# Kernel optimization log

Hardware: AMD Instinct MI355X
Metric: run time of the kernel (lower is better)

Reference implementation:

```python
import jax, jax.numpy as jnp
import numpy as np

D = 1024      # hidden_size
M = 256       # num_random_features
N = 16384     # number of hidden states
K = 8192      # number of weight rows (HSM nodes)
EPS = 1e-6


def _orthogonal_random_features(key, d, m):
    # m < d: single QR block, first m rows, scaled by sqrt(d)
    rm = jax.random.normal(key, (d, d), dtype=jnp.float32)
    q, _ = jnp.linalg.qr(rm)
    return q[:m] * jnp.sqrt(jnp.float32(d))


def setup_inputs() -> dict:
    key = jax.random.key(0)
    k1, k2, k3 = jax.random.split(key, 3)
    hidden_states = jax.random.normal(k1, (N, D), dtype=jnp.float32)
    weights = jax.random.normal(k2, (K, D), dtype=jnp.float32)
    omega = _orthogonal_random_features(k3, D, M)
    return {"hidden_states": hidden_states, "weights": weights, "omega": omega}


def _positive_random_features(x, omega):
    # phi(x) = (exp(x @ Omega^T - ||x||^2/2 - max) + eps) / sqrt(m)
    projection = x @ omega.T                                  # (..., m)
    x_norm_sq = jnp.sum(x * x, axis=-1, keepdims=True)        # (..., 1)
    exponent = projection - x_norm_sq / 2
    exponent_max = jnp.max(exponent, axis=-1, keepdims=True)
    features = (jnp.exp(exponent - exponent_max) + EPS) / jnp.sqrt(jnp.float32(omega.shape[0]))
    return features, x_norm_sq, exponent_max


def reference(hidden_states, weights, omega):
    # temperature = 1.0 (default), so no input rescaling
    phi_h, h_norm_sq, h_max = _positive_random_features(hidden_states, omega)  # (n,m)
    phi_w, w_norm_sq, w_max = _positive_random_features(weights, omega)        # (k,m)
    rf_kernel = phi_h @ phi_w.T                                                # (n,k)
    log_correction = (h_norm_sq + w_norm_sq.T) / 2 + h_max + w_max.T           # (n,k)
    log_correction = jnp.clip(log_correction, -80.0, 80.0)
    log_rf_kernel = jnp.log(rf_kernel + 1e-10)
    log_exp_approx = jnp.clip(log_rf_kernel + log_correction, -80.0, 80.0)
    exp_approx = jnp.exp(log_exp_approx)
    return exp_approx / (1.0 + exp_approx)
```

## Files before the change

### kernel.cpp

```cpp
#include <hip/hip_runtime.h>

#define DD 1024
#define MM 256
#define NN 16384
#define KK 8192

typedef float f32x4 __attribute__((ext_vector_type(4)));
typedef unsigned int u32x4 __attribute__((ext_vector_type(4)));
typedef unsigned int u32x2 __attribute__((ext_vector_type(2)));
typedef __bf16 bf16x8 __attribute__((ext_vector_type(8)));
typedef unsigned short u16;
typedef unsigned int u32;

static __device__ __forceinline__ u16 f2bf(float f) {
    u32 u = __builtin_bit_cast(u32, f);
    u32 r = u + 0x7fffu + ((u >> 16) & 1u);
    return (u16)(r >> 16);
}
static __device__ __forceinline__ float bf2f(u16 h) {
    u32 u = ((u32)h) << 16;
    return __builtin_bit_cast(float, u);
}

static __device__ __forceinline__ void gload_lds16(const void* g, void* l) {
    __builtin_amdgcn_global_load_lds(
        (const __attribute__((address_space(1))) u32*)g,
        (__attribute__((address_space(3))) u32*)l, 16, 0, 0);
}

static __device__ __forceinline__ bf16x8 ldfrag(const u16* p) {
    return __builtin_bit_cast(bf16x8, *(const u32x4*)p);
}

#define MFMA16(a, b, c) __builtin_amdgcn_mfma_f32_16x16x32_bf16((a), (b), (c), 0, 0, 0)

__global__ void k_conv(const float* __restrict__ om, u16* __restrict__ oh,
                       u16* __restrict__ ol) {
    int i = (blockIdx.x * blockDim.x + threadIdx.x) * 4;
    f32x4 x = *(const f32x4*)(om + i);
    ushort4 h, l;
    u16 t;
    t = f2bf(x.x); h.x = t; l.x = f2bf(x.x - bf2f(t));
    t = f2bf(x.y); h.y = t; l.y = f2bf(x.y - bf2f(t));
    t = f2bf(x.z); h.z = t; l.z = f2bf(x.z - bf2f(t));
    t = f2bf(x.w); h.w = t; l.w = f2bf(x.w - bf2f(t));
    *(ushort4*)(oh + i) = h;
    *(ushort4*)(ol + i) = l;
}

__global__ __launch_bounds__(256, 4)
void k_stageA(const float* __restrict__ Hs, const float* __restrict__ Ws,
              const u16* __restrict__ Oh, const u16* __restrict__ Ol,
              u16* __restrict__ phiH, u16* __restrict__ phiW,
              float* __restrict__ emH, float* __restrict__ emW)
{
    __shared__ alignas(16) u16 Ah[32 * 32];
    __shared__ alignas(16) u16 Al[32 * 32];
    __shared__ alignas(16) u16 Bh[256 * 32];
    __shared__ alignas(16) u16 Bl[256 * 32];
    __shared__ float redmax[4][32];

    const int tid  = threadIdx.x;
    const int lane = tid & 63;
    const int wid  = tid >> 6;

    const float* __restrict__ X;
    u16* __restrict__ phi;
    float* __restrict__ em;
    int row0;
    if (blockIdx.x < NN / 32) {
        X = Hs; phi = phiH; em = emH; row0 = blockIdx.x * 32;
    } else {
        X = Ws; phi = phiW; em = emW; row0 = (blockIdx.x - NN / 32) * 32;
    }

    f32x4 acc[2][4];
#pragma unroll
    for (int m = 0; m < 2; ++m)
#pragma unroll
        for (int n = 0; n < 4; ++n) acc[m][n] = f32x4{0.f, 0.f, 0.f, 0.f};

    const int arow = tid >> 3;
    const int acol = (tid & 7) * 4;
    const float* __restrict__ xrow = X + (long)(row0 + arow) * DD;
    const int a_idx = arow * 32 + (acol ^ (((arow >> 1) & 3) << 3));

    const int r16 = lane & 15;
    const int h8  = (lane >> 4) << 3;
    int aoffs[2], boffs[4];
#pragma unroll
    for (int m = 0; m < 2; ++m) {
        int row = m * 16 + r16;
        aoffs[m] = row * 32 + (h8 ^ (((row >> 1) & 3) << 3));
    }
#pragma unroll
    for (int n = 0; n < 4; ++n) {
        int row = wid * 64 + n * 16 + r16;
        boffs[n] = row * 32 + (h8 ^ (((row >> 1) & 3) << 3));
    }

    for (int ks = 0; ks < DD / 32; ++ks) {
        const int k0 = ks * 32;
#pragma unroll
        for (int s = 0; s < 4; ++s) {
            const int c    = s * 256 + tid;
            const int brow = c >> 2;
            const int scol = k0 + (((c & 3) << 3) ^ (((brow >> 1) & 3) << 3));
            gload_lds16(Oh + brow * DD + scol, Bh + (s * 256 + wid * 64) * 8);
            gload_lds16(Ol + brow * DD + scol, Bl + (s * 256 + wid * 64) * 8);
        }
        f32x4 x = *(const f32x4*)(xrow + k0 + acol);
        u32x2 ph, pl;
#pragma unroll
        for (int j = 0; j < 2; ++j) {
            u16 h0 = f2bf(x[2 * j]);
            u16 h1 = f2bf(x[2 * j + 1]);
            u16 l0 = f2bf(x[2 * j] - bf2f(h0));
            u16 l1 = f2bf(x[2 * j + 1] - bf2f(h1));
            ph[j] = (u32)h0 | ((u32)h1 << 16);
            pl[j] = (u32)l0 | ((u32)l1 << 16);
        }
        *(u32x2*)(Ah + a_idx) = ph;
        *(u32x2*)(Al + a_idx) = pl;
        __syncthreads();

        bf16x8 fah[2], fal[2], fbh[4], fbl[4];
#pragma unroll
        for (int m = 0; m < 2; ++m) {
            fah[m] = ldfrag(Ah + aoffs[m]);
            fal[m] = ldfrag(Al + aoffs[m]);
        }
#pragma unroll
        for (int n = 0; n < 4; ++n) {
            fbh[n] = ldfrag(Bh + boffs[n]);
            fbl[n] = ldfrag(Bl + boffs[n]);
        }
#pragma unroll
        for (int m = 0; m < 2; ++m)
#pragma unroll
            for (int n = 0; n < 4; ++n) {
                acc[m][n] = MFMA16(fah[m], fbh[n], acc[m][n]);
                acc[m][n] = MFMA16(fah[m], fbl[n], acc[m][n]);
                acc[m][n] = MFMA16(fal[m], fbh[n], acc[m][n]);
            }
        __syncthreads();
    }

#pragma unroll
    for (int m = 0; m < 2; ++m) {
#pragma unroll
        for (int i = 0; i < 4; ++i) {
            float v = fmaxf(fmaxf(acc[m][0][i], acc[m][1][i]),
                            fmaxf(acc[m][2][i], acc[m][3][i]));
            v = fmaxf(v, __shfl_xor(v, 1));
            v = fmaxf(v, __shfl_xor(v, 2));
            v = fmaxf(v, __shfl_xor(v, 4));
            v = fmaxf(v, __shfl_xor(v, 8));
            if (r16 == 0) redmax[wid][m * 16 + ((lane >> 4) << 2) + i] = v;
        }
    }
    __syncthreads();
    if (tid < 32) {
        float fm = fmaxf(fmaxf(redmax[0][tid], redmax[1][tid]),
                         fmaxf(redmax[2][tid], redmax[3][tid]));
        em[row0 + tid] = __expf(fminf(fmaxf(-fm, -87.f), 87.f));
    }
#pragma unroll
    for (int m = 0; m < 2; ++m) {
#pragma unroll
        for (int i = 0; i < 4; ++i) {
            const int rl = m * 16 + ((lane >> 4) << 2) + i;
            const float fm = fmaxf(fmaxf(redmax[0][rl], redmax[1][rl]),
                                   fmaxf(redmax[2][rl], redmax[3][rl]));
#pragma unroll
            for (int n = 0; n < 4; ++n) {
                float p   = acc[m][n][i];
                float ph_ = (__expf(p - fm) + 1e-6f) * 0.0625f;
                phi[(long)(row0 + rl) * MM + wid * 64 + n * 16 + r16] = f2bf(ph_);
            }
        }
    }
}

__global__ __launch_bounds__(256, 3)
void k_stageB(const u16* __restrict__ PH, const u16* __restrict__ PW,
              const float* __restrict__ EH, const float* __restrict__ EW,
              float* __restrict__ out)
{
    __shared__ alignas(16) u16 As[128 * 64];
    __shared__ alignas(16) u16 Bs[128 * 64];

    const int tid  = threadIdx.x;
    const int lane = tid & 63;
    const int wid  = tid >> 6;
    const int bm   = blockIdx.x >> 6;
    const int bn   = blockIdx.x & 63;
    const int row0 = bm * 128, col0 = bn * 128;
    const int wr   = wid >> 1, wc = wid & 1;
    const int r16  = lane & 15;
    const int h8   = (lane >> 4) << 3;

    f32x4 acc[4][4];
#pragma unroll
    for (int m = 0; m < 4; ++m)
#pragma unroll
        for (int n = 0; n < 4; ++n) acc[m][n] = f32x4{0.f, 0.f, 0.f, 0.f};

    int aoffs[2][4], boffs[2][4];
#pragma unroll
    for (int sl = 0; sl < 2; ++sl) {
#pragma unroll
        for (int m = 0; m < 4; ++m) {
            int row = wr * 64 + m * 16 + r16;
            aoffs[sl][m] = row * 64 + (((((sl * 32 + h8) << 1)) ^ ((row & 7) << 4)) >> 1);
        }
#pragma unroll
        for (int n = 0; n < 4; ++n) {
            int row = wc * 64 + n * 16 + r16;
            boffs[sl][n] = row * 64 + (((((sl * 32 + h8) << 1)) ^ ((row & 7) << 4)) >> 1);
        }
    }

    for (int ks = 0; ks < 4; ++ks) {
        const int k0 = ks * 64;
#pragma unroll
        for (int s = 0; s < 4; ++s) {
            const int c    = s * 256 + tid;
            const int row  = c >> 3;
            const int cbl  = ((c & 7) << 4) ^ ((row & 7) << 4);
            const int scol = k0 + (cbl >> 1);
            gload_lds16(PH + (long)(row0 + row) * MM + scol, As + (s * 256 + wid * 64) * 8);
            gload_lds16(PW + (long)(col0 + row) * MM + scol, Bs + (s * 256 + wid * 64) * 8);
        }
        __syncthreads();
#pragma unroll
        for (int sl = 0; sl < 2; ++sl) {
            bf16x8 fa[4], fb[4];
#pragma unroll
            for (int m = 0; m < 4; ++m) fa[m] = ldfrag(As + aoffs[sl][m]);
#pragma unroll
            for (int n = 0; n < 4; ++n) fb[n] = ldfrag(Bs + boffs[sl][n]);
#pragma unroll
            for (int m = 0; m < 4; ++m)
#pragma unroll
                for (int n = 0; n < 4; ++n)
                    acc[m][n] = MFMA16(fa[m], fb[n], acc[m][n]);
        }
        __syncthreads();
    }

    float ew_[4];
#pragma unroll
    for (int n = 0; n < 4; ++n) ew_[n] = EW[col0 + wc * 64 + n * 16 + r16];

#pragma unroll
    for (int m = 0; m < 4; ++m) {
#pragma unroll
        for (int i = 0; i < 4; ++i) {
            const int row = row0 + wr * 64 + m * 16 + ((lane >> 4) << 2) + i;
            const float eh = EH[row];
#pragma unroll
            for (int n = 0; n < 4; ++n) {
                float rf = acc[m][n][i] + 1e-10f;
                float t  = eh * ew_[n];
                float o  = rf * __builtin_amdgcn_rcpf(rf + t);
                __builtin_nontemporal_store(
                    o, &out[(long)row * KK + col0 + wc * 64 + n * 16 + r16]);
            }
        }
    }
}

extern "C" void kernel_launch(void* const* d_in, const int* in_sizes, int n_in,
                              void* d_out, int out_size, void* d_ws, size_t ws_size,
                              hipStream_t stream) {
    (void)in_sizes; (void)n_in; (void)out_size; (void)ws_size;
    const float* H  = (const float*)d_in[0];
    const float* W  = (const float*)d_in[1];
    const float* Om = (const float*)d_in[2];
    float* out = (float*)d_out;

    char* ws   = (char*)d_ws;
    u16*  phiH = (u16*)ws;
    u16*  phiW = (u16*)(ws + (size_t)NN * MM * 2);
    float* emh = (float*)(ws + (size_t)(NN + KK) * MM * 2);
    float* emw = emh + NN;
    u16*  oh   = (u16*)(emw + KK);
    u16*  ol   = oh + MM * DD;

    k_conv<<<(MM * DD) / 1024, 256, 0, stream>>>(Om, oh, ol);
    k_stageA<<<(NN + KK) / 32, 256, 0, stream>>>(H, W, oh, ol, phiH, phiW, emh, emw);
    k_stageB<<<(NN / 128) * (KK / 128), 256, 0, stream>>>(phiH, phiW, emh, emw, out);
}
```

Baseline: 196.3 us.

## Double-buffer both GEMM stages, load A fragments directly, swizzle stage B tiles

Stage A now double-buffers the omega tiles in LDS and prefetches the next hidden-state slice into registers while the current one is computed. The hidden rows are split to bf16 hi/lo directly into MFMA fragments without an LDS round trip, and hidden-state blocks cover 64 rows instead of 32. Stage B double-buffers its LDS tiles so global loads overlap the MFMAs, and remaps block indices so concurrently running blocks share rows for L2 reuse. Both kernels lower their launch_bounds occupancy hint to 2 and use more LDS per block, trading occupancy for overlap.

```diff
diff --git a/kernel.cpp b/kernel.cpp
--- a/kernel.cpp
+++ b/kernel.cpp
@@ -7,7 +7,6 @@
 
 typedef float f32x4 __attribute__((ext_vector_type(4)));
 typedef unsigned int u32x4 __attribute__((ext_vector_type(4)));
-typedef unsigned int u32x2 __attribute__((ext_vector_type(2)));
 typedef __bf16 bf16x8 __attribute__((ext_vector_type(8)));
 typedef unsigned short u16;
 typedef unsigned int u32;
@@ -48,106 +47,115 @@
     *(ushort4*)(ol + i) = l;
 }
 
-__global__ __launch_bounds__(256, 4)
-void k_stageA(const float* __restrict__ Hs, const float* __restrict__ Ws,
-              const u16* __restrict__ Oh, const u16* __restrict__ Ol,
-              u16* __restrict__ phiH, u16* __restrict__ phiW,
-              float* __restrict__ emH, float* __restrict__ emW)
+template<int MT>
+static __device__ __forceinline__ void stageA_body(
+    const float* __restrict__ X,
+    const u16* __restrict__ Oh, const u16* __restrict__ Ol,
+    u16* __restrict__ phi, float* __restrict__ em, int row0,
+    u16* __restrict__ Bh0, u16* __restrict__ Bl0,
+    u16* __restrict__ Bh1, u16* __restrict__ Bl1,
+    float (*redmax)[64])
 {
-    __shared__ alignas(16) u16 Ah[32 * 32];
-    __shared__ alignas(16) u16 Al[32 * 32];
-    __shared__ alignas(16) u16 Bh[256 * 32];
-    __shared__ alignas(16) u16 Bl[256 * 32];
-    __shared__ float redmax[4][32];
-
     const int tid  = threadIdx.x;
     const int lane = tid & 63;
     const int wid  = tid >> 6;
-
-    const float* __restrict__ X;
-    u16* __restrict__ phi;
-    float* __restrict__ em;
-    int row0;
-    if (blockIdx.x < NN / 32) {
-        X = Hs; phi = phiH; em = emH; row0 = blockIdx.x * 32;
-    } else {
-        X = Ws; phi = phiW; em = emW; row0 = (blockIdx.x - NN / 32) * 32;
-    }
-
-    f32x4 acc[2][4];
-#pragma unroll
-    for (int m = 0; m < 2; ++m)
+    const int r16  = lane & 15;
+    const int h8   = (lane >> 4) << 3;
+
+    f32x4 acc[MT][4];
+#pragma unroll
+    for (int m = 0; m < MT; ++m)
 #pragma unroll
         for (int n = 0; n < 4; ++n) acc[m][n] = f32x4{0.f, 0.f, 0.f, 0.f};
 
-    const int arow = tid >> 3;
-    const int acol = (tid & 7) * 4;
-    const float* __restrict__ xrow = X + (long)(row0 + arow) * DD;
-    const int a_idx = arow * 32 + (acol ^ (((arow >> 1) & 3) << 3));
-
-    const int r16 = lane & 15;
-    const int h8  = (lane >> 4) << 3;
-    int aoffs[2], boffs[4];
-#pragma unroll
-    for (int m = 0; m < 2; ++m) {
-        int row = m * 16 + r16;
-        aoffs[m] = row * 32 + (h8 ^ (((row >> 1) & 3) << 3));
-    }
+    int boffs[4];
 #pragma unroll
     for (int n = 0; n < 4; ++n) {
         int row = wid * 64 + n * 16 + r16;
         boffs[n] = row * 32 + (h8 ^ (((row >> 1) & 3) << 3));
     }
 
-    for (int ks = 0; ks < DD / 32; ++ks) {
+    const float* xb[MT];
+#pragma unroll
+    for (int m = 0; m < MT; ++m)
+        xb[m] = X + (long)(row0 + m * 16 + r16) * DD + h8;
+
+    u32x4 xr0[MT][2], xr1[MT][2];
+
+    auto stage = [&](int ks, u16* bh, u16* bl) {
         const int k0 = ks * 32;
 #pragma unroll
         for (int s = 0; s < 4; ++s) {
             const int c    = s * 256 + tid;
             const int brow = c >> 2;
             const int scol = k0 + (((c & 3) << 3) ^ (((brow >> 1) & 3) << 3));
-            gload_lds16(Oh + brow * DD + scol, Bh + (s * 256 + wid * 64) * 8);
-            gload_lds16(Ol + brow * DD + scol, Bl + (s * 256 + wid * 64) * 8);
-        }
-        f32x4 x = *(const f32x4*)(xrow + k0 + acol);
-        u32x2 ph, pl;
-#pragma unroll
-        for (int j = 0; j < 2; ++j) {
-            u16 h0 = f2bf(x[2 * j]);
-            u16 h1 = f2bf(x[2 * j + 1]);
-            u16 l0 = f2bf(x[2 * j] - bf2f(h0));
-            u16 l1 = f2bf(x[2 * j + 1] - bf2f(h1));
-            ph[j] = (u32)h0 | ((u32)h1 << 16);
-            pl[j] = (u32)l0 | ((u32)l1 << 16);
-        }
-        *(u32x2*)(Ah + a_idx) = ph;
-        *(u32x2*)(Al + a_idx) = pl;
-        __syncthreads();
-
-        bf16x8 fah[2], fal[2], fbh[4], fbl[4];
-#pragma unroll
-        for (int m = 0; m < 2; ++m) {
-            fah[m] = ldfrag(Ah + aoffs[m]);
-            fal[m] = ldfrag(Al + aoffs[m]);
+            gload_lds16(Oh + brow * DD + scol, bh + (s * 256 + wid * 64) * 8);
+            gload_lds16(Ol + brow * DD + scol, bl + (s * 256 + wid * 64) * 8);
+        }
+    };
+    auto loadA = [&](int ks, u32x4 (&xr)[MT][2]) {
+        const int k0 = ks * 32;
+#pragma unroll
+        for (int m = 0; m < MT; ++m) {
+            xr[m][0] = *(const u32x4*)(xb[m] + k0);
+            xr[m][1] = *(const u32x4*)(xb[m] + k0 + 4);
+        }
+    };
+    auto compute = [&](u32x4 (&xr)[MT][2], const u16* bh, const u16* bl) {
+        bf16x8 fah[MT], fal[MT], fbh[4], fbl[4];
+#pragma unroll
+        for (int m = 0; m < MT; ++m) {
+            f32x4 a = __builtin_bit_cast(f32x4, xr[m][0]);
+            f32x4 b = __builtin_bit_cast(f32x4, xr[m][1]);
+            const float p0[4] = {a[0], a[2], b[0], b[2]};
+            const float p1[4] = {a[1], a[3], b[1], b[3]};
+            u32x4 ph, pl;
+#pragma unroll
+            for (int j = 0; j < 4; ++j) {
+                u16 h0 = f2bf(p0[j]);
+                u16 h1 = f2bf(p1[j]);
+                u16 l0 = f2bf(p0[j] - bf2f(h0));
+                u16 l1 = f2bf(p1[j] - bf2f(h1));
+                ph[j] = (u32)h0 | ((u32)h1 << 16);
+                pl[j] = (u32)l0 | ((u32)l1 << 16);
+            }
+            fah[m] = __builtin_bit_cast(bf16x8, ph);
+            fal[m] = __builtin_bit_cast(bf16x8, pl);
         }
 #pragma unroll
         for (int n = 0; n < 4; ++n) {
-            fbh[n] = ldfrag(Bh + boffs[n]);
-            fbl[n] = ldfrag(Bl + boffs[n]);
-        }
-#pragma unroll
-        for (int m = 0; m < 2; ++m)
+            fbh[n] = ldfrag(bh + boffs[n]);
+            fbl[n] = ldfrag(bl + boffs[n]);
+        }
+#pragma unroll
+        for (int m = 0; m < MT; ++m)
 #pragma unroll
             for (int n = 0; n < 4; ++n) {
                 acc[m][n] = MFMA16(fah[m], fbh[n], acc[m][n]);
                 acc[m][n] = MFMA16(fah[m], fbl[n], acc[m][n]);
                 acc[m][n] = MFMA16(fal[m], fbh[n], acc[m][n]);
             }
+    };
+
+    stage(0, Bh0, Bl0);
+    loadA(0, xr0);
+    __syncthreads();
+
+    for (int ks = 0; ks < 32; ks += 2) {
+        stage(ks + 1, Bh1, Bl1);
+        loadA(ks + 1, xr1);
+        compute(xr0, Bh0, Bl0);
         __syncthreads();
-    }
-
-#pragma unroll
-    for (int m = 0; m < 2; ++m) {
+        if (ks + 2 < 32) {
+            stage(ks + 2, Bh0, Bl0);
+            loadA(ks + 2, xr0);
+        }
+        compute(xr1, Bh1, Bl1);
+        __syncthreads();
+    }
+
+#pragma unroll
+    for (int m = 0; m < MT; ++m)
 #pragma unroll
         for (int i = 0; i < 4; ++i) {
             float v = fmaxf(fmaxf(acc[m][0][i], acc[m][1][i]),
@@ -158,15 +166,14 @@
             v = fmaxf(v, __shfl_xor(v, 8));
             if (r16 == 0) redmax[wid][m * 16 + ((lane >> 4) << 2) + i] = v;
         }
-    }
     __syncthreads();
-    if (tid < 32) {
+    if (tid < MT * 16) {
         float fm = fmaxf(fmaxf(redmax[0][tid], redmax[1][tid]),
                          fmaxf(redmax[2][tid], redmax[3][tid]));
         em[row0 + tid] = __expf(fminf(fmaxf(-fm, -87.f), 87.f));
     }
 #pragma unroll
-    for (int m = 0; m < 2; ++m) {
+    for (int m = 0; m < MT; ++m)
 #pragma unroll
         for (int i = 0; i < 4; ++i) {
             const int rl = m * 16 + ((lane >> 4) << 2) + i;
@@ -179,22 +186,39 @@
                 phi[(long)(row0 + rl) * MM + wid * 64 + n * 16 + r16] = f2bf(ph_);
             }
         }
-    }
-}
-
-__global__ __launch_bounds__(256, 3)
+}
+
+__global__ __launch_bounds__(256, 2)
+void k_stageA(const float* __restrict__ Hs, const float* __restrict__ Ws,
+              const u16* __restrict__ Oh, const u16* __restrict__ Ol,
+              u16* __restrict__ phiH, u16* __restrict__ phiW,
+              float* __restrict__ emH, float* __restrict__ emW)
+{
+    __shared__ alignas(16) u16 Bh[2][256 * 32];
+    __shared__ alignas(16) u16 Bl[2][256 * 32];
+    __shared__ float redmax[4][64];
+    if (blockIdx.x < NN / 64)
+        stageA_body<4>(Hs, Oh, Ol, phiH, emH, blockIdx.x * 64,
+                       Bh[0], Bl[0], Bh[1], Bl[1], redmax);
+    else
+        stageA_body<2>(Ws, Oh, Ol, phiW, emW, (blockIdx.x - NN / 64) * 32,
+                       Bh[0], Bl[0], Bh[1], Bl[1], redmax);
+}
+
+__global__ __launch_bounds__(256, 2)
 void k_stageB(const u16* __restrict__ PH, const u16* __restrict__ PW,
               const float* __restrict__ EH, const float* __restrict__ EW,
               float* __restrict__ out)
 {
-    __shared__ alignas(16) u16 As[128 * 64];
-    __shared__ alignas(16) u16 Bs[128 * 64];
+    __shared__ alignas(16) u16 As[2][128 * 64];
+    __shared__ alignas(16) u16 Bs[2][128 * 64];
 
     const int tid  = threadIdx.x;
     const int lane = tid & 63;
     const int wid  = tid >> 6;
-    const int bm   = blockIdx.x >> 6;
-    const int bn   = blockIdx.x & 63;
+    const int swz  = (blockIdx.x & 7) * 1024 + (blockIdx.x >> 3);
+    const int bm   = swz >> 6;
+    const int bn   = swz & 63;
     const int row0 = bm * 128, col0 = bn * 128;
     const int wr   = wid >> 1, wc = wid & 1;
     const int r16  = lane & 15;
@@ -212,34 +236,43 @@
 #pragma unroll
         for (int m = 0; m < 4; ++m) {
             int row = wr * 64 + m * 16 + r16;
-            aoffs[sl][m] = row * 64 + (((((sl * 32 + h8) << 1)) ^ ((row & 7) << 4)) >> 1);
+            aoffs[sl][m] = row * 64 + ((sl * 32 + h8) ^ ((row & 7) << 3));
         }
 #pragma unroll
         for (int n = 0; n < 4; ++n) {
             int row = wc * 64 + n * 16 + r16;
-            boffs[sl][n] = row * 64 + (((((sl * 32 + h8) << 1)) ^ ((row & 7) << 4)) >> 1);
-        }
-    }
-
-    for (int ks = 0; ks < 4; ++ks) {
+            boffs[sl][n] = row * 64 + ((sl * 32 + h8) ^ ((row & 7) << 3));
+        }
+    }
+
+    auto stage = [&](int ks, int b) {
         const int k0 = ks * 64;
 #pragma unroll
         for (int s = 0; s < 4; ++s) {
             const int c    = s * 256 + tid;
             const int row  = c >> 3;
-            const int cbl  = ((c & 7) << 4) ^ ((row & 7) << 4);
-            const int scol = k0 + (cbl >> 1);
-            gload_lds16(PH + (long)(row0 + row) * MM + scol, As + (s * 256 + wid * 64) * 8);
-            gload_lds16(PW + (long)(col0 + row) * MM + scol, Bs + (s * 256 + wid * 64) * 8);
-        }
-        __syncthreads();
+            const int scol = k0 + (((c & 7) << 3) ^ ((row & 7) << 3));
+            gload_lds16(PH + (long)(row0 + row) * MM + scol,
+                        &As[b][(s * 256 + wid * 64) * 8]);
+            gload_lds16(PW + (long)(col0 + row) * MM + scol,
+                        &Bs[b][(s * 256 + wid * 64) * 8]);
+        }
+    };
+
+    stage(0, 0);
+    __syncthreads();
+
+#pragma unroll
+    for (int ks = 0; ks < 4; ++ks) {
+        const int b = ks & 1;
+        if (ks < 3) stage(ks + 1, b ^ 1);
 #pragma unroll
         for (int sl = 0; sl < 2; ++sl) {
             bf16x8 fa[4], fb[4];
 #pragma unroll
-            for (int m = 0; m < 4; ++m) fa[m] = ldfrag(As + aoffs[sl][m]);
-#pragma unroll
-            for (int n = 0; n < 4; ++n) fb[n] = ldfrag(Bs + boffs[sl][n]);
+            for (int m = 0; m < 4; ++m) fa[m] = ldfrag(&As[b][0] + aoffs[sl][m]);
+#pragma unroll
+            for (int n = 0; n < 4; ++n) fb[n] = ldfrag(&Bs[b][0] + boffs[sl][n]);
 #pragma unroll
             for (int m = 0; m < 4; ++m)
 #pragma unroll
@@ -289,6 +322,6 @@
     u16*  ol   = oh + MM * DD;
 
     k_conv<<<(MM * DD) / 1024, 256, 0, stream>>>(Om, oh, ol);
-    k_stageA<<<(NN + KK) / 32, 256, 0, stream>>>(H, W, oh, ol, phiH, phiW, emh, emw);
+    k_stageA<<<NN / 64 + KK / 32, 256, 0, stream>>>(H, W, oh, ol, phiH, phiW, emh, emw);
     k_stageB<<<(NN / 128) * (KK / 128), 256, 0, stream>>>(phiH, phiW, emh, emw, out);
 }
```

New measurement: 253.1 us. 1.29x slower.

## Make stage A per-wave with register-prefetched X and no block barriers

Applied to the files above, without the earlier changes.

Stage A now gives each wave a private LDS slice of the omega tile and loads the hidden-state A fragments straight from global memory into registers, splitting them into bf16 hi/lo there. Nothing is shared between waves, so the two __syncthreads per K-step go away. The next step's omega tile and X values are prefetched into a double-buffered register set before the current step's MFMAs are issued. The cost is more registers, so launch bounds drop from 4 to 3 waves, and each wave now reads X on its own. The correctness of the in-place LDS reuse depends on the hand-placed s_waitcnt ordering.

```diff
diff --git a/kernel.cpp b/kernel.cpp
--- a/kernel.cpp
+++ b/kernel.cpp
@@ -7,7 +7,6 @@
 
 typedef float f32x4 __attribute__((ext_vector_type(4)));
 typedef unsigned int u32x4 __attribute__((ext_vector_type(4)));
-typedef unsigned int u32x2 __attribute__((ext_vector_type(2)));
 typedef __bf16 bf16x8 __attribute__((ext_vector_type(8)));
 typedef unsigned short u16;
 typedef unsigned int u32;
@@ -48,21 +47,21 @@
     *(ushort4*)(ol + i) = l;
 }
 
-__global__ __launch_bounds__(256, 4)
+__global__ __launch_bounds__(256, 3)
 void k_stageA(const float* __restrict__ Hs, const float* __restrict__ Ws,
               const u16* __restrict__ Oh, const u16* __restrict__ Ol,
               u16* __restrict__ phiH, u16* __restrict__ phiW,
               float* __restrict__ emH, float* __restrict__ emW)
 {
-    __shared__ alignas(16) u16 Ah[32 * 32];
-    __shared__ alignas(16) u16 Al[32 * 32];
-    __shared__ alignas(16) u16 Bh[256 * 32];
-    __shared__ alignas(16) u16 Bl[256 * 32];
+    __shared__ alignas(16) u16 BhS[4][64 * 32];
+    __shared__ alignas(16) u16 BlS[4][64 * 32];
     __shared__ float redmax[4][32];
 
     const int tid  = threadIdx.x;
     const int lane = tid & 63;
     const int wid  = tid >> 6;
+    const int r16  = lane & 15;
+    const int h8   = (lane >> 4) << 3;
 
     const float* __restrict__ X;
     u16* __restrict__ phi;
@@ -80,60 +79,78 @@
 #pragma unroll
         for (int n = 0; n < 4; ++n) acc[m][n] = f32x4{0.f, 0.f, 0.f, 0.f};
 
-    const int arow = tid >> 3;
-    const int acol = (tid & 7) * 4;
-    const float* __restrict__ xrow = X + (long)(row0 + arow) * DD;
-    const int a_idx = arow * 32 + (acol ^ (((arow >> 1) & 3) << 3));
-
-    const int r16 = lane & 15;
-    const int h8  = (lane >> 4) << 3;
-    int aoffs[2], boffs[4];
-#pragma unroll
-    for (int m = 0; m < 2; ++m) {
-        int row = m * 16 + r16;
-        aoffs[m] = row * 32 + (h8 ^ (((row >> 1) & 3) << 3));
-    }
+    u16* const mybh = &BhS[wid][0];
+    u16* const mybl = &BlS[wid][0];
+
+    int boffs[4];
 #pragma unroll
     for (int n = 0; n < 4; ++n) {
-        int row = wid * 64 + n * 16 + r16;
-        boffs[n] = row * 32 + (h8 ^ (((row >> 1) & 3) << 3));
-    }
-
-    for (int ks = 0; ks < DD / 32; ++ks) {
-        const int k0 = ks * 32;
+        int rl = n * 16 + r16;
+        boffs[n] = rl * 32 + (h8 ^ (((rl >> 1) & 3) << 3));
+    }
+
+    const u16* srch[4];
+    const u16* srcl[4];
+#pragma unroll
+    for (int s = 0; s < 4; ++s) {
+        int rl  = s * 16 + (lane >> 2);
+        int col = ((lane & 3) << 3) ^ (((rl >> 1) & 3) << 3);
+        srch[s] = Oh + (long)(wid * 64 + rl) * DD + col;
+        srcl[s] = Ol + (long)(wid * 64 + rl) * DD + col;
+    }
+
+    const float* xb[2];
+#pragma unroll
+    for (int m = 0; m < 2; ++m)
+        xb[m] = X + (long)(row0 + m * 16 + r16) * DD + h8;
+
+    u32x4 xrA[2][2], xrB[2][2];
+
+    auto stageO = [&](int k0) {
 #pragma unroll
         for (int s = 0; s < 4; ++s) {
-            const int c    = s * 256 + tid;
-            const int brow = c >> 2;
-            const int scol = k0 + (((c & 3) << 3) ^ (((brow >> 1) & 3) << 3));
-            gload_lds16(Oh + brow * DD + scol, Bh + (s * 256 + wid * 64) * 8);
-            gload_lds16(Ol + brow * DD + scol, Bl + (s * 256 + wid * 64) * 8);
-        }
-        f32x4 x = *(const f32x4*)(xrow + k0 + acol);
-        u32x2 ph, pl;
-#pragma unroll
-        for (int j = 0; j < 2; ++j) {
-            u16 h0 = f2bf(x[2 * j]);
-            u16 h1 = f2bf(x[2 * j + 1]);
-            u16 l0 = f2bf(x[2 * j] - bf2f(h0));
-            u16 l1 = f2bf(x[2 * j + 1] - bf2f(h1));
-            ph[j] = (u32)h0 | ((u32)h1 << 16);
-            pl[j] = (u32)l0 | ((u32)l1 << 16);
-        }
-        *(u32x2*)(Ah + a_idx) = ph;
-        *(u32x2*)(Al + a_idx) = pl;
-        __syncthreads();
-
-        bf16x8 fah[2], fal[2], fbh[4], fbl[4];
+            gload_lds16(srch[s] + k0, mybh + s * 512);
+            gload_lds16(srcl[s] + k0, mybl + s * 512);
+        }
+    };
+    auto loadX = [&](int k0, u32x4 (&xr)[2][2]) {
 #pragma unroll
         for (int m = 0; m < 2; ++m) {
-            fah[m] = ldfrag(Ah + aoffs[m]);
-            fal[m] = ldfrag(Al + aoffs[m]);
-        }
+            xr[m][0] = *(const u32x4*)(xb[m] + k0);
+            xr[m][1] = *(const u32x4*)(xb[m] + k0 + 4);
+        }
+    };
+    auto step = [&](u32x4 (&xr)[2][2], u32x4 (&xrn)[2][2], int k_next) {
+        asm volatile("s_waitcnt vmcnt(0)" ::: "memory");
+        bf16x8 fbh[4], fbl[4];
 #pragma unroll
         for (int n = 0; n < 4; ++n) {
-            fbh[n] = ldfrag(Bh + boffs[n]);
-            fbl[n] = ldfrag(Bl + boffs[n]);
+            fbh[n] = ldfrag(mybh + boffs[n]);
+            fbl[n] = ldfrag(mybl + boffs[n]);
+        }
+        bf16x8 fah[2], fal[2];
+#pragma unroll
+        for (int m = 0; m < 2; ++m) {
+            f32x4 a = __builtin_bit_cast(f32x4, xr[m][0]);
+            f32x4 b = __builtin_bit_cast(f32x4, xr[m][1]);
+            const float e[8] = {a[0], a[1], a[2], a[3], b[0], b[1], b[2], b[3]};
+            u32x4 ph, pl;
+#pragma unroll
+            for (int j = 0; j < 4; ++j) {
+                u16 h0 = f2bf(e[2 * j]);
+                u16 h1 = f2bf(e[2 * j + 1]);
+                u16 l0 = f2bf(e[2 * j] - bf2f(h0));
+                u16 l1 = f2bf(e[2 * j + 1] - bf2f(h1));
+                ph[j] = (u32)h0 | ((u32)h1 << 16);
+                pl[j] = (u32)l0 | ((u32)l1 << 16);
+            }
+            fah[m] = __builtin_bit_cast(bf16x8, ph);
+            fal[m] = __builtin_bit_cast(bf16x8, pl);
+        }
+        asm volatile("s_waitcnt lgkmcnt(0)" ::: "memory");
+        if (k_next < DD) {
+            stageO(k_next);
+            loadX(k_next, xrn);
         }
 #pragma unroll
         for (int m = 0; m < 2; ++m)
@@ -143,11 +160,18 @@
                 acc[m][n] = MFMA16(fah[m], fbl[n], acc[m][n]);
                 acc[m][n] = MFMA16(fal[m], fbh[n], acc[m][n]);
             }
-        __syncthreads();
-    }
-
-#pragma unroll
-    for (int m = 0; m < 2; ++m) {
+    };
+
+    stageO(0);
+    loadX(0, xrA);
+
+    for (int ks = 0; ks < 32; ks += 2) {
+        step(xrA, xrB, (ks + 1) * 32);
+        step(xrB, xrA, (ks + 2) * 32);
+    }
+
+#pragma unroll
+    for (int m = 0; m < 2; ++m)
 #pragma unroll
         for (int i = 0; i < 4; ++i) {
             float v = fmaxf(fmaxf(acc[m][0][i], acc[m][1][i]),
@@ -158,7 +182,6 @@
             v = fmaxf(v, __shfl_xor(v, 8));
             if (r16 == 0) redmax[wid][m * 16 + ((lane >> 4) << 2) + i] = v;
         }
-    }
     __syncthreads();
     if (tid < 32) {
         float fm = fmaxf(fmaxf(redmax[0][tid], redmax[1][tid]),
@@ -166,7 +189,7 @@
         em[row0 + tid] = __expf(fminf(fmaxf(-fm, -87.f), 87.f));
     }
 #pragma unroll
-    for (int m = 0; m < 2; ++m) {
+    for (int m = 0; m < 2; ++m)
 #pragma unroll
         for (int i = 0; i < 4; ++i) {
             const int rl = m * 16 + ((lane >> 4) << 2) + i;
@@ -179,7 +202,6 @@
                 phi[(long)(row0 + rl) * MM + wid * 64 + n * 16 + r16] = f2bf(ph_);
             }
         }
-    }
 }
 
 __global__ __launch_bounds__(256, 3)
```

New measurement: 211.2 us. 7.6% more time.
